# Kernel optimization log

Measured on AMD Instinct MI355X. Metric: run time of the kernel, lower is better.

The kernel has to match this reference:

```python
import jax, jax.numpy as jnp
import numpy as np

N_NODES = 100000
HIDDEN = 128
E = 524288  # edges per graph (pos and neg)


def setup_inputs() -> dict:
    key = jax.random.key(0)
    ks = jax.random.split(key, 8)
    return {
        "z_src": jax.random.normal(ks[0], (N_NODES, HIDDEN), dtype=jnp.float32),
        "z_dst": jax.random.normal(ks[1], (N_NODES, HIDDEN), dtype=jnp.float32),
        "pos_src": jax.random.randint(ks[2], (E,), 0, N_NODES, dtype=jnp.int64),
        "pos_dst": jax.random.randint(ks[3], (E,), 0, N_NODES, dtype=jnp.int64),
        "neg_src": jax.random.randint(ks[4], (E,), 0, N_NODES, dtype=jnp.int64),
        "neg_dst": jax.random.randint(ks[5], (E,), 0, N_NODES, dtype=jnp.int64),
        "W1": jax.random.normal(ks[6], (2 * HIDDEN, HIDDEN), dtype=jnp.float32) * (1.0 / np.sqrt(2 * HIDDEN)),
        "b1": jnp.zeros((HIDDEN,), dtype=jnp.float32),
        "W2": jax.random.normal(ks[7], (HIDDEN, 1), dtype=jnp.float32) * (1.0 / np.sqrt(HIDDEN)),
        "b2": jnp.zeros((1,), dtype=jnp.float32),
    }


def reference(z_src, z_dst, pos_src, pos_dst, neg_src, neg_dst, W1, b1, W2, b2):
    # Gather endpoint features for pos then neg edges (cat along edge dim)
    src_idx = jnp.concatenate([pos_src, neg_src])  # [2E]
    dst_idx = jnp.concatenate([pos_dst, neg_dst])  # [2E]
    z = jnp.concatenate([z_src[src_idx], z_dst[dst_idx]], axis=-1)  # [2E, 2h]
    z = jax.nn.relu(z @ W1 + b1)  # [2E, h]
    z = z @ W2 + b2               # [2E, 1]
    return z.reshape(-1)
```

## Files before the change

### kernel.cpp

```cpp
#include <hip/hip_runtime.h>
#include <hip/hip_bf16.h>
#include <cstdint>

#define N_NODES 100000
#define HIDDEN  128
#define NEDGE   524288

typedef __attribute__((ext_vector_type(8))) short short8;
typedef __attribute__((ext_vector_type(4))) float f32x4;

__device__ __forceinline__ unsigned short f2b(float f) {
    unsigned u = __float_as_uint(f);
    u += 0x7FFFu + ((u >> 16) & 1u);
    return (unsigned short)(u >> 16);
}
__device__ __forceinline__ float b2f(unsigned x16) {
    return __uint_as_float(x16 << 16);
}

__global__ __launch_bounds__(256, 3)
void precompute_kernel(const float* __restrict__ z_src,
                       const float* __restrict__ z_dst,
                       const float* __restrict__ W1,
                       unsigned short* __restrict__ Asrc,
                       unsigned short* __restrict__ Adst)
{
    const int table = blockIdx.y;
    const float* z = table ? z_dst : z_src;
    const float* W = W1 + table * (128 * 128);
    unsigned short* A = table ? Adst : Asrc;

    __shared__ unsigned short lds_wt[128 * 136];
    __shared__ unsigned short lds_z[64 * 136];

    const int tid = threadIdx.x;

    for (int idx = tid; idx < 128 * 128; idx += 256) {
        int k = idx >> 7, n = idx & 127;
        lds_wt[n * 136 + k] = f2b(W[k * 128 + n]);
    }

    const int wave = tid >> 6;
    const int lane = tid & 63;
    const int t = lane & 15;
    const int q = lane >> 4;

    for (int it = 0; it < 4; ++it) {
        const int m0 = (blockIdx.x * 4 + it) * 64;
        if (m0 >= N_NODES) break;
        __syncthreads();

        for (int idx = tid; idx < 64 * 32; idx += 256) {
            int r = idx >> 5, c4 = idx & 31;
            int row = m0 + r;
            float4 v = make_float4(0.f, 0.f, 0.f, 0.f);
            if (row < N_NODES) v = *(const float4*)(z + (size_t)row * 128 + c4 * 4);
            ushort4 h;
            h.x = f2b(v.x); h.y = f2b(v.y); h.z = f2b(v.z); h.w = f2b(v.w);
            *(ushort4*)&lds_z[r * 136 + c4 * 4] = h;
        }
        __syncthreads();

        f32x4 acc[8];
#pragma unroll
        for (int n = 0; n < 8; ++n) acc[n] = (f32x4){0.f, 0.f, 0.f, 0.f};

#pragma unroll
        for (int ks = 0; ks < 4; ++ks) {
            const int k0 = ks * 32;
            short8 a = *(const short8*)&lds_z[(wave * 16 + t) * 136 + k0 + q * 8];
#pragma unroll
            for (int n = 0; n < 8; ++n) {
                short8 b = *(const short8*)&lds_wt[(n * 16 + t) * 136 + k0 + q * 8];
                acc[n] = __builtin_amdgcn_mfma_f32_16x16x32_bf16(a, b, acc[n], 0, 0, 0);
            }
        }

#pragma unroll
        for (int n = 0; n < 8; ++n) {
#pragma unroll
            for (int r = 0; r < 4; ++r) {
                int row = m0 + wave * 16 + q * 4 + r;
                if (row < N_NODES)
                    A[(size_t)row * 128 + n * 16 + t] = f2b(acc[n][r]);
            }
        }
    }
}

__global__ __launch_bounds__(256, 6)
void edge_kernel(const unsigned short* __restrict__ Asrc,
                 const unsigned short* __restrict__ Adst,
                 const int* __restrict__ pos_src,
                 const int* __restrict__ pos_dst,
                 const int* __restrict__ neg_src,
                 const int* __restrict__ neg_dst,
                 const float* __restrict__ b1,
                 const float* __restrict__ W2,
                 const float* __restrict__ b2,
                 float* __restrict__ out)
{
    const int tid = threadIdx.x;
    const int t = tid & 15;
    const int g = tid >> 4;

    float b1r[8], w2r[8];
#pragma unroll
    for (int j = 0; j < 8; ++j) {
        b1r[j] = b1[t * 8 + j];
        w2r[j] = W2[t * 8 + j];
    }
    const float bias2 = b2[0];

    const int ebase = blockIdx.x * 128;
#pragma unroll 2
    for (int i = 0; i < 8; ++i) {
        const int e = ebase + i * 16 + g;
        int s, d;
        if (e < NEDGE) { s = pos_src[e]; d = pos_dst[e]; }
        else           { s = neg_src[e - NEDGE]; d = neg_dst[e - NEDGE]; }

        const uint4 ua = *(const uint4*)(Asrc + (size_t)s * 128 + t * 8);
        const uint4 ub = *(const uint4*)(Adst + (size_t)d * 128 + t * 8);

        float acc = 0.f;
        const unsigned* pa = (const unsigned*)&ua;
        const unsigned* pb = (const unsigned*)&ub;
#pragma unroll
        for (int j2 = 0; j2 < 4; ++j2) {
            float h0 = b2f(pa[j2] & 0xFFFFu) + b2f(pb[j2] & 0xFFFFu) + b1r[2 * j2];
            float h1 = b2f(pa[j2] >> 16)     + b2f(pb[j2] >> 16)     + b1r[2 * j2 + 1];
            h0 = fmaxf(h0, 0.f);
            h1 = fmaxf(h1, 0.f);
            acc = fmaf(h0, w2r[2 * j2], acc);
            acc = fmaf(h1, w2r[2 * j2 + 1], acc);
        }
        acc += __shfl_xor(acc, 1);
        acc += __shfl_xor(acc, 2);
        acc += __shfl_xor(acc, 4);
        acc += __shfl_xor(acc, 8);
        if (t == 0) out[e] = acc + bias2;
    }
}

extern "C" void kernel_launch(void* const* d_in, const int* in_sizes, int n_in,
                              void* d_out, int out_size, void* d_ws, size_t ws_size,
                              hipStream_t stream) {
    const float* z_src  = (const float*)d_in[0];
    const float* z_dst  = (const float*)d_in[1];
    const int* pos_src  = (const int*)d_in[2];
    const int* pos_dst  = (const int*)d_in[3];
    const int* neg_src  = (const int*)d_in[4];
    const int* neg_dst  = (const int*)d_in[5];
    const float* W1     = (const float*)d_in[6];
    const float* b1     = (const float*)d_in[7];
    const float* W2     = (const float*)d_in[8];
    const float* b2     = (const float*)d_in[9];
    float* out = (float*)d_out;

    unsigned short* Asrc = (unsigned short*)d_ws;
    unsigned short* Adst = Asrc + (size_t)N_NODES * HIDDEN;

    dim3 pgrid(391, 2);
    precompute_kernel<<<pgrid, 256, 0, stream>>>(z_src, z_dst, W1, Asrc, Adst);

    edge_kernel<<<8192, 256, 0, stream>>>(Asrc, Adst, pos_src, pos_dst,
                                          neg_src, neg_dst, b1, W2, b2, out);
}
```

Measured before the change: 251.6 us.

## Pretranspose W1 once, drop LDS staging in precompute, batch edge gathers

Adds a small kernel that transposes and converts W1 to bf16 once. The precompute kernel then reads z rows and weights straight from global memory into MFMA operands, with no LDS staging or barriers, and swaps operand roles so each lane writes a contiguous ushort4. The edge kernel picks the pos or neg index array per block and issues all 8 index loads and all 16 row gathers before computing, to raise memory-level parallelism. The costs are an extra launch, higher register pressure (occupancy hint lowered to 4), and repeated global reads of the weights in place of LDS reuse.

```diff
diff --git a/kernel.cpp b/kernel.cpp
--- a/kernel.cpp
+++ b/kernel.cpp
@@ -18,77 +18,70 @@
     return __uint_as_float(x16 << 16);
 }
 
-__global__ __launch_bounds__(256, 3)
+__global__ void wt_kernel(const float* __restrict__ W1,
+                          unsigned short* __restrict__ Wt)
+{
+    const int row = blockIdx.x;
+    const int n = row & 127;
+    const int tb = row >> 7;
+    const int k = threadIdx.x;
+    Wt[(size_t)row * 128 + k] = f2b(W1[(size_t)(tb * 128 + k) * 128 + n]);
+}
+
+__global__ __launch_bounds__(256, 4)
 void precompute_kernel(const float* __restrict__ z_src,
                        const float* __restrict__ z_dst,
-                       const float* __restrict__ W1,
+                       const unsigned short* __restrict__ Wt,
                        unsigned short* __restrict__ Asrc,
                        unsigned short* __restrict__ Adst)
 {
     const int table = blockIdx.y;
     const float* z = table ? z_dst : z_src;
-    const float* W = W1 + table * (128 * 128);
+    const unsigned short* W = Wt + table * (128 * 128);
     unsigned short* A = table ? Adst : Asrc;
 
-    __shared__ unsigned short lds_wt[128 * 136];
-    __shared__ unsigned short lds_z[64 * 136];
-
-    const int tid = threadIdx.x;
-
-    for (int idx = tid; idx < 128 * 128; idx += 256) {
-        int k = idx >> 7, n = idx & 127;
-        lds_wt[n * 136 + k] = f2b(W[k * 128 + n]);
-    }
-
-    const int wave = tid >> 6;
-    const int lane = tid & 63;
+    const int wave = threadIdx.x >> 6;
+    const int lane = threadIdx.x & 63;
     const int t = lane & 15;
     const int q = lane >> 4;
 
-    for (int it = 0; it < 4; ++it) {
-        const int m0 = (blockIdx.x * 4 + it) * 64;
-        if (m0 >= N_NODES) break;
-        __syncthreads();
+    const int m0 = (blockIdx.x * 4 + wave) * 16;
+    if (m0 >= N_NODES) return;
 
-        for (int idx = tid; idx < 64 * 32; idx += 256) {
-            int r = idx >> 5, c4 = idx & 31;
-            int row = m0 + r;
-            float4 v = make_float4(0.f, 0.f, 0.f, 0.f);
-            if (row < N_NODES) v = *(const float4*)(z + (size_t)row * 128 + c4 * 4);
-            ushort4 h;
-            h.x = f2b(v.x); h.y = f2b(v.y); h.z = f2b(v.z); h.w = f2b(v.w);
-            *(ushort4*)&lds_z[r * 136 + c4 * 4] = h;
-        }
-        __syncthreads();
+    const float* zrow = z + (size_t)(m0 + t) * 128;
 
-        f32x4 acc[8];
+    f32x4 acc[8];
 #pragma unroll
-        for (int n = 0; n < 8; ++n) acc[n] = (f32x4){0.f, 0.f, 0.f, 0.f};
+    for (int n = 0; n < 8; ++n) acc[n] = (f32x4){0.f, 0.f, 0.f, 0.f};
 
 #pragma unroll
-        for (int ks = 0; ks < 4; ++ks) {
-            const int k0 = ks * 32;
-            short8 a = *(const short8*)&lds_z[(wave * 16 + t) * 136 + k0 + q * 8];
-#pragma unroll
-            for (int n = 0; n < 8; ++n) {
-                short8 b = *(const short8*)&lds_wt[(n * 16 + t) * 136 + k0 + q * 8];
-                acc[n] = __builtin_amdgcn_mfma_f32_16x16x32_bf16(a, b, acc[n], 0, 0, 0);
-            }
-        }
-
+    for (int ks = 0; ks < 4; ++ks) {
+        const int k0 = ks * 32 + q * 8;
+        const float4 v0 = *(const float4*)(zrow + k0);
+        const float4 v1 = *(const float4*)(zrow + k0 + 4);
+        short8 b;
+        b[0] = (short)f2b(v0.x); b[1] = (short)f2b(v0.y);
+        b[2] = (short)f2b(v0.z); b[3] = (short)f2b(v0.w);
+        b[4] = (short)f2b(v1.x); b[5] = (short)f2b(v1.y);
+        b[6] = (short)f2b(v1.z); b[7] = (short)f2b(v1.w);
 #pragma unroll
         for (int n = 0; n < 8; ++n) {
+            const short8 a = *(const short8*)(W + (size_t)(n * 16 + t) * 128 + k0);
+            acc[n] = __builtin_amdgcn_mfma_f32_16x16x32_bf16(a, b, acc[n], 0, 0, 0);
+        }
+    }
+
+    unsigned short* arow = A + (size_t)(m0 + t) * 128;
 #pragma unroll
-            for (int r = 0; r < 4; ++r) {
-                int row = m0 + wave * 16 + q * 4 + r;
-                if (row < N_NODES)
-                    A[(size_t)row * 128 + n * 16 + t] = f2b(acc[n][r]);
-            }
-        }
+    for (int n = 0; n < 8; ++n) {
+        ushort4 h;
+        h.x = f2b(acc[n][0]); h.y = f2b(acc[n][1]);
+        h.z = f2b(acc[n][2]); h.w = f2b(acc[n][3]);
+        *(ushort4*)(arow + n * 16 + q * 4) = h;
     }
 }
 
-__global__ __launch_bounds__(256, 6)
+__global__ __launch_bounds__(256, 4)
 void edge_kernel(const unsigned short* __restrict__ Asrc,
                  const unsigned short* __restrict__ Adst,
                  const int* __restrict__ pos_src,
@@ -104,6 +97,11 @@
     const int t = tid & 15;
     const int g = tid >> 4;
 
+    const bool is_pos = blockIdx.x < 4096;
+    const int* __restrict__ sp = is_pos ? pos_src : neg_src;
+    const int* __restrict__ dp = is_pos ? pos_dst : neg_dst;
+    const int eb = (is_pos ? blockIdx.x : blockIdx.x - 4096) * 128;
+
     float b1r[8], w2r[8];
 #pragma unroll
     for (int j = 0; j < 8; ++j) {
@@ -112,20 +110,25 @@
     }
     const float bias2 = b2[0];
 
-    const int ebase = blockIdx.x * 128;
-#pragma unroll 2
+    int sidx[8], didx[8];
+#pragma unroll
     for (int i = 0; i < 8; ++i) {
-        const int e = ebase + i * 16 + g;
-        int s, d;
-        if (e < NEDGE) { s = pos_src[e]; d = pos_dst[e]; }
-        else           { s = neg_src[e - NEDGE]; d = neg_dst[e - NEDGE]; }
+        sidx[i] = sp[eb + i * 16 + g];
+        didx[i] = dp[eb + i * 16 + g];
+    }
 
-        const uint4 ua = *(const uint4*)(Asrc + (size_t)s * 128 + t * 8);
-        const uint4 ub = *(const uint4*)(Adst + (size_t)d * 128 + t * 8);
+    uint4 ua[8], ub[8];
+#pragma unroll
+    for (int i = 0; i < 8; ++i) {
+        ua[i] = *(const uint4*)(Asrc + (size_t)sidx[i] * 128 + t * 8);
+        ub[i] = *(const uint4*)(Adst + (size_t)didx[i] * 128 + t * 8);
+    }
 
+#pragma unroll
+    for (int i = 0; i < 8; ++i) {
         float acc = 0.f;
-        const unsigned* pa = (const unsigned*)&ua;
-        const unsigned* pb = (const unsigned*)&ub;
+        const unsigned* pa = (const unsigned*)&ua[i];
+        const unsigned* pb = (const unsigned*)&ub[i];
 #pragma unroll
         for (int j2 = 0; j2 < 4; ++j2) {
             float h0 = b2f(pa[j2] & 0xFFFFu) + b2f(pb[j2] & 0xFFFFu) + b1r[2 * j2];
@@ -139,7 +142,7 @@
         acc += __shfl_xor(acc, 2);
         acc += __shfl_xor(acc, 4);
         acc += __shfl_xor(acc, 8);
-        if (t == 0) out[e] = acc + bias2;
+        if (t == 0) out[blockIdx.x * 128 + i * 16 + g] = acc + bias2;
     }
 }
 
@@ -160,9 +163,12 @@
 
     unsigned short* Asrc = (unsigned short*)d_ws;
     unsigned short* Adst = Asrc + (size_t)N_NODES * HIDDEN;
+    unsigned short* Wt   = Adst + (size_t)N_NODES * HIDDEN;
 
-    dim3 pgrid(391, 2);
-    precompute_kernel<<<pgrid, 256, 0, stream>>>(z_src, z_dst, W1, Asrc, Adst);
+    wt_kernel<<<256, 128, 0, stream>>>(W1, Wt);
+
+    dim3 pgrid(1563, 2);
+    precompute_kernel<<<pgrid, 256, 0, stream>>>(z_src, z_dst, Wt, Asrc, Adst);
 
     edge_kernel<<<8192, 256, 0, stream>>>(Asrc, Adst, pos_src, pos_dst,
                                           neg_src, neg_dst, b1, W2, b2, out);
```

Result: slower. 258.7 us (+2.8%).
